# Optimization experiments

Hardware: AMD Instinct MI355X
Metric: run time of the kernel (lower is better)

## Reference

```python
import jax, jax.numpy as jnp
import numpy as np

B, T, IN, H, NC = 128, 256, 512, 1024, 10


def setup_inputs() -> dict:
    key = jax.random.key(0)
    ks = jax.random.split(key, 18)
    s = jnp.float32(0.05)

    def n(k, shape):
        return jax.random.normal(k, shape, dtype=jnp.float32) * s

    inp = {"x": n(ks[0], (B, T, IN))}
    in_dims = [IN, H, H]
    ki = 1
    for l in range(3):
        inp[f"w_ih{l}"] = n(ks[ki], (4 * H, in_dims[l])); ki += 1
        inp[f"w_hh{l}"] = n(ks[ki], (4 * H, H)); ki += 1
        inp[f"b_ih{l}"] = n(ks[ki], (4 * H,)); ki += 1
        inp[f"b_hh{l}"] = n(ks[ki], (4 * H,)); ki += 1
    inp["w1"] = n(ks[ki], (32, H)); ki += 1
    inp["b1"] = n(ks[ki], (32,)); ki += 1
    inp["w2"] = n(ks[ki], (NC, 32)); ki += 1
    inp["b2"] = n(ks[ki], (NC,))
    return inp


def _lstm_layer(xs, w_ih, w_hh, b):
    # xs: [B, T, D_in]; PyTorch gate order i, f, g, o
    bsz = xs.shape[0]
    hid = w_hh.shape[1]
    # Precompute input projection for all timesteps (one big GEMM)
    xp = jnp.einsum('bti,gi->btg', xs, w_ih) + b  # [B, T, 4H]

    def step(carry, xp_t):
        h, c = carry
        gates = xp_t + h @ w_hh.T  # [B, 4H]
        i, f, g, o = jnp.split(gates, 4, axis=-1)
        c = jax.nn.sigmoid(f) * c + jax.nn.sigmoid(i) * jnp.tanh(g)
        h = jax.nn.sigmoid(o) * jnp.tanh(c)
        return (h, c), h

    h0 = jnp.zeros((bsz, hid), xs.dtype)
    c0 = jnp.zeros((bsz, hid), xs.dtype)
    (_, _), hs = jax.lax.scan(step, (h0, c0), jnp.swapaxes(xp, 0, 1))
    return jnp.swapaxes(hs, 0, 1)  # [B, T, H]


def reference(x, w_ih0, w_hh0, b_ih0, b_hh0,
              w_ih1, w_hh1, b_ih1, b_hh1,
              w_ih2, w_hh2, b_ih2, b_hh2,
              w1, b1, w2, b2):
    h = x
    layers = [(w_ih0, w_hh0, b_ih0, b_hh0),
              (w_ih1, w_hh1, b_ih1, b_hh1),
              (w_ih2, w_hh2, b_ih2, b_hh2)]
    for w_ih, w_hh, b_ih, b_hh in layers:
        h = _lstm_layer(h, w_ih, w_hh, b_ih + b_hh)
    last = h[:, -1, :]                      # [B, H]
    hid = jax.nn.relu(last @ w1.T + b1)     # [B, 32]
    return hid @ w2.T + b2                  # [B, NC]
```

## Files before the change

kernel.cpp:

```cpp
#include <hip/hip_runtime.h>
#include <hip/hip_bf16.h>
#include <stdint.h>

#define B_ 128
#define T_ 256
#define IN_ 512
#define H_ 1024
#define G4_ 4096
#define TC_ 64
#define NCHUNK_ (T_ / TC_)

typedef __bf16 bf16x8 __attribute__((ext_vector_type(8)));
typedef float f32x4 __attribute__((ext_vector_type(4)));
typedef uint32_t u32x4 __attribute__((ext_vector_type(4)));

#define AS1U(p) ((const __attribute__((address_space(1))) unsigned int*)(p))
#define AS3U(p) ((__attribute__((address_space(3))) unsigned int*)(p))

__device__ __forceinline__ uint16_t f2bf(float f) {
  union { float f; uint32_t u; } v; v.f = f;
  uint32_t r = (v.u + 0x7fffu + ((v.u >> 16) & 1u)) >> 16;
  return (uint16_t)r;
}
__device__ __forceinline__ float bf2f(uint16_t h) {
  union { uint32_t u; float f; } v; v.u = ((uint32_t)h) << 16;
  return v.f;
}
__device__ __forceinline__ float sigmoid_f(float x) {
  return 1.f / (1.f + __expf(-x));
}
__device__ __forceinline__ float tanh_f(float x) {
  x = fminf(15.f, fmaxf(-15.f, x));
  float e = __expf(2.f * x);
  return (e - 1.f) / (e + 1.f);
}

__global__ void k_f32_to_bf16(const float* __restrict__ src, uint16_t* __restrict__ dst, int n) {
  int i = (blockIdx.x * blockDim.x + threadIdx.x) * 4;
  if (i >= n) return;
  float4 v = *(const float4*)(src + i);
  ushort4 o;
  o.x = f2bf(v.x); o.y = f2bf(v.y); o.z = f2bf(v.z); o.w = f2bf(v.w);
  *(ushort4*)(dst + i) = o;
}

__global__ void k_bias(const float* __restrict__ a, const float* __restrict__ b, float* __restrict__ o) {
  int i = blockIdx.x * blockDim.x + threadIdx.x;
  if (i < G4_) o[i] = a[i] + b[i];
}

__global__ void k_whh_frag(const float* __restrict__ whh, uint16_t* __restrict__ dst) {
  int t = blockIdx.x * blockDim.x + threadIdx.x;
  int lane = t & 63;
  int kk = (t >> 6) & 15;
  int w  = (t >> 10) & 15;
  int s5 = t >> 14;
  int nt = w & 7, kh = w >> 3;
  int row = (nt >> 1) * 1024 + s5 * 32 + (nt & 1) * 16 + (lane & 15);
  int col = kh * 512 + kk * 32 + ((lane >> 4) << 3);
  const float* sp = whh + (size_t)row * H_ + col;
  uint16_t o[8];
  #pragma unroll
  for (int j = 0; j < 8; ++j) o[j] = f2bf(sp[j]);
  uint4 pk;
  __builtin_memcpy(&pk, o, 16);
  *(uint4*)(dst + (size_t)t * 8) = pk;
}

__global__ __launch_bounds__(256, 1) void k_gemm_xp(
    const uint16_t* __restrict__ A, const uint16_t* __restrict__ W,
    const float* __restrict__ bias, uint16_t* __restrict__ xp,
    int K, int t0)
{
  __shared__ __align__(16) char smem[128 * 136 * 2];
  uint16_t* As = (uint16_t*)smem;
  uint16_t* Bs = (uint16_t*)(smem + 32768 / 2 * 2 - 16384);
  uint16_t* Cs = (uint16_t*)smem;
  const int tid = threadIdx.x;
  const int l = tid & 63;
  const int w = tid >> 6;
  const int mx = blockIdx.x;
  const int n0 = blockIdx.y * 128;
  const int wm = (w >> 1) * 64;
  const int wn = (w & 1) * 64;

  f32x4 acc[4][4] = {};

  for (int k0 = 0; k0 < K; k0 += 32) {
    __syncthreads();
    #pragma unroll
    for (int it = 0; it < 2; ++it) {
      const int chunk = w * 2 + it;
      const int loff = chunk * 1024 + l * 16;
      const int row = loff >> 6;
      const int colb = loff & 63;
      const int gm = mx * 512 + t0 + ((row >> 6) << 8) + (row & 63);
      const uint16_t* ga = A + (size_t)gm * K + k0 + (colb >> 1);
      __builtin_amdgcn_global_load_lds(AS1U(ga), AS3U((char*)As + chunk * 1024), 16, 0, 0);
      const uint16_t* gb = W + (size_t)(n0 + row) * K + k0 + (colb >> 1);
      __builtin_amdgcn_global_load_lds(AS1U(gb), AS3U((char*)Bs + chunk * 1024), 16, 0, 0);
    }
    __syncthreads();
    bf16x8 af[4], bfr[4];
    #pragma unroll
    for (int i = 0; i < 4; ++i)
      af[i] = *(const bf16x8*)&As[(wm + i * 16 + (l & 15)) * 32 + ((l >> 4) << 3)];
    #pragma unroll
    for (int j = 0; j < 4; ++j)
      bfr[j] = *(const bf16x8*)&Bs[(wn + j * 16 + (l & 15)) * 32 + ((l >> 4) << 3)];
    #pragma unroll
    for (int i = 0; i < 4; ++i) {
      #pragma unroll
      for (int j = 0; j < 4; ++j)
        acc[i][j] = __builtin_amdgcn_mfma_f32_16x16x32_bf16(af[i], bfr[j], acc[i][j], 0, 0, 0);
    }
  }
  __syncthreads();

  #pragma unroll
  for (int i = 0; i < 4; ++i) {
    const int row = wm + i * 16 + ((l >> 4) << 2);
    #pragma unroll
    for (int j = 0; j < 4; ++j) {
      const int col = wn + j * 16 + (l & 15);
      const float bv = bias[n0 + col];
      #pragma unroll
      for (int r = 0; r < 4; ++r)
        Cs[(row + r) * 136 + col] = f2bf(acc[i][j][r] + bv);
    }
  }
  __syncthreads();
  #pragma unroll
  for (int it = 0; it < 8; ++it) {
    const int row = it * 16 + w * 4 + (l >> 4);
    uint4 v = *(const uint4*)&Cs[row * 136 + (l & 15) * 8];
    *(uint4*)(xp + (size_t)(mx * 128 + row) * G4_ + n0 + (l & 15) * 8) = v;
  }
}

__global__ __launch_bounds__(1024, 4) void k_lstm(
    const uint16_t* __restrict__ whhf, const uint16_t* __restrict__ xp,
    uint16_t* __restrict__ seq, uint32_t* __restrict__ hbuf,
    float* __restrict__ cbuf, unsigned int* __restrict__ flags, int t0, int sall)
{
  __shared__ __align__(16) uint16_t Astg[2048 * 8];
  __shared__ float part[2][8][16][17];
  const int tid = threadIdx.x;
  const int l = tid & 63;
  const int w = tid >> 6;
  const int nt = w & 7;
  const int kh = w >> 3;
  const int bid = blockIdx.x;
  const int g = bid & 7;
  const int s5 = bid >> 3;
  const int U0 = s5 * 32;
  const int gs0 = g * 16;

  unsigned int* gflag = flags + g * 32;

  bf16x8 bfr[16];
  {
    const uint16_t* wp = whhf + (size_t)(s5 * 16 + w) * 8192 + l * 8;
    #pragma unroll
    for (int kk = 0; kk < 16; ++kk)
      bfr[kk] = *(const bf16x8*)(wp + kk * 512);
  }

  const int u = tid & 31;
  const int smg = (tid >> 5) & 15;
  float cc = 0.f;
  if (tid < 512) cc = cbuf[(size_t)(gs0 + smg) * H_ + U0 + u];

  uint16_t x0 = 0, x1 = 0, x2 = 0, x3 = 0;
  if (tid < 512) {
    const uint16_t* p = xp + ((size_t)(gs0 + smg) * TC_ + 0) * G4_ + U0 + u;
    x0 = p[0]; x1 = p[1024]; x2 = p[2048]; x3 = p[3072];
  }

  auto stage_fused = [&](int tl) {
    const int par = tl & 1;
    const unsigned tgt = (unsigned)tl;
    const char* src = (const char*)hbuf + (size_t)par * (B_ * H_ * 2)
                      + (size_t)(gs0 + w) * 2048 + (size_t)l * 32;
    const unsigned int* fp = gflag + (l >> 1);
    u32x4 q0, q1;
    unsigned fv;
    do {
      asm volatile(
        "global_load_dword %0, %3, off sc0 sc1\n\t"
        "global_load_dwordx4 %1, %4, off sc0 sc1\n\t"
        "global_load_dwordx4 %2, %4, off offset:16 sc0 sc1\n\t"
        "s_waitcnt vmcnt(0)"
        : "=&v"(fv), "=&v"(q0), "=&v"(q1)
        : "v"(fp), "v"(src)
        : "memory");
      if (fv >= tgt) break;
      __builtin_amdgcn_s_sleep(1);
    } while (true);
    const int base = 512 * l + ((w ^ (l & 7)) << 4);
    *(u32x4*)((char*)Astg + base) = q0;
    *(u32x4*)((char*)Astg + base + 256) = q1;
  };

  stage_fused(0);
  __syncthreads();

  for (int tl = 0; tl < TC_; ++tl) {
    const int par = tl & 1;

    f32x4 e0 = {0.f, 0.f, 0.f, 0.f};
    f32x4 e1 = {0.f, 0.f, 0.f, 0.f};
    #pragma unroll
    for (int kk = 0; kk < 16; kk += 2) {
      const int c0 = kh * 64 + kk * 4 + (l >> 4);
      const int c1 = c0 + 4;
      const int sw0 = (l & 15) ^ ((2 * kk + (l >> 5)) & 7);
      const int sw1 = (l & 15) ^ ((2 * (kk + 1) + (l >> 5)) & 7);
      bf16x8 a0 = *(const bf16x8*)((const char*)Astg + ((size_t)(c0 * 16 + sw0) << 4));
      bf16x8 a1 = *(const bf16x8*)((const char*)Astg + ((size_t)(c1 * 16 + sw1) << 4));
      e0 = __builtin_amdgcn_mfma_f32_16x16x32_bf16(a0, bfr[kk],     e0, 0, 0, 0);
      e1 = __builtin_amdgcn_mfma_f32_16x16x32_bf16(a1, bfr[kk + 1], e1, 0, 0, 0);
    }
    f32x4 e = e0 + e1;
    #pragma unroll
    for (int r = 0; r < 4; ++r)
      part[kh][nt][((l >> 4) << 2) + r][l & 15] = e[r];
    __syncthreads();

    if (tid < 512) {
      const int sub = u >> 4, uc = u & 15;
      float gi = part[0][0 + sub][smg][uc] + part[1][0 + sub][smg][uc] + bf2f(x0);
      float gf = part[0][2 + sub][smg][uc] + part[1][2 + sub][smg][uc] + bf2f(x1);
      float gg = part[0][4 + sub][smg][uc] + part[1][4 + sub][smg][uc] + bf2f(x2);
      float go = part[0][6 + sub][smg][uc] + part[1][6 + sub][smg][uc] + bf2f(x3);
      cc = sigmoid_f(gf) * cc + sigmoid_f(gi) * tanh_f(gg);
      float hh = sigmoid_f(go) * tanh_f(cc);
      uint16_t hb = f2bf(hh);
      unsigned int o = (unsigned int)__shfl_xor((int)(unsigned int)hb, 1);
      if ((u & 1) == 0) {
        uint32_t pk = (uint32_t)hb | (o << 16);
        const int b = gs0 + smg;
        uint32_t* hp = hbuf + (size_t)(1 - par) * (B_ * H_ / 2)
                            + ((size_t)b * H_ + U0 + u) / 2;
        __hip_atomic_store(hp, pk, __ATOMIC_RELAXED, __HIP_MEMORY_SCOPE_SYSTEM);
        if (sall || (t0 + tl == T_ - 1)) {
          uint32_t* sq = (uint32_t*)seq + (((size_t)b * T_ + (t0 + tl)) * H_ + U0 + u) / 2;
          *sq = pk;
        }
      }
      if (tl + 1 < TC_) {
        const uint16_t* p = xp + ((size_t)(gs0 + smg) * TC_ + tl + 1) * G4_ + U0 + u;
        x0 = p[0]; x1 = p[1024]; x2 = p[2048]; x3 = p[3072];
      }
    }
    __syncthreads();
    if (tid == 0)
      __hip_atomic_store(gflag + s5, (unsigned)(tl + 1),
                         __ATOMIC_RELAXED, __HIP_MEMORY_SCOPE_SYSTEM);
    if (tl + 1 < TC_) {
      stage_fused(tl + 1);
      __syncthreads();
    }
  }
  if (tid < 512) cbuf[(size_t)(gs0 + smg) * H_ + U0 + u] = cc;
}

__global__ __launch_bounds__(256) void k_mlp(
    const uint16_t* __restrict__ seq2,
    const float* __restrict__ w1, const float* __restrict__ b1,
    const float* __restrict__ w2, const float* __restrict__ b2,
    float* __restrict__ out)
{
  __shared__ float hv[H_];
  __shared__ float part[32][8];
  __shared__ float hid[32];
  const int b = blockIdx.x, tid = threadIdx.x;
  const uint16_t* hrow = seq2 + ((size_t)b * T_ + (T_ - 1)) * H_;
  for (int i = tid; i < H_; i += 256) hv[i] = bf2f(hrow[i]);
  __syncthreads();
  const int j = tid >> 3, p = tid & 7;
  float sum = 0.f;
  const float* wr = w1 + (size_t)j * H_ + p * 128;
  const float* hp = hv + p * 128;
  for (int k = 0; k < 128; ++k) sum += wr[k] * hp[k];
  part[j][p] = sum;
  __syncthreads();
  if (tid < 32) {
    float s2 = 0.f;
    #pragma unroll
    for (int pp = 0; pp < 8; ++pp) s2 += part[tid][pp];
    hid[tid] = fmaxf(s2 + b1[tid], 0.f);
  }
  __syncthreads();
  if (tid < 10) {
    float o = b2[tid];
    #pragma unroll
    for (int jj = 0; jj < 32; ++jj) o += hid[jj] * w2[tid * 32 + jj];
    out[b * 10 + tid] = o;
  }
}

extern "C" void kernel_launch(void* const* d_in, const int* in_sizes, int n_in,
                              void* d_out, int out_size, void* d_ws, size_t ws_size,
                              hipStream_t stream)
{
  const float* x = (const float*)d_in[0];
  const float* w_ih[3] = {(const float*)d_in[1], (const float*)d_in[5], (const float*)d_in[9]};
  const float* w_hh[3] = {(const float*)d_in[2], (const float*)d_in[6], (const float*)d_in[10]};
  const float* b_ih[3] = {(const float*)d_in[3], (const float*)d_in[7], (const float*)d_in[11]};
  const float* b_hh[3] = {(const float*)d_in[4], (const float*)d_in[8], (const float*)d_in[12]};
  const float* w1 = (const float*)d_in[13];
  const float* b1 = (const float*)d_in[14];
  const float* w2 = (const float*)d_in[15];
  const float* b2 = (const float*)d_in[16];
  float* out = (float*)d_out;

  char* ws = (char*)d_ws;
  size_t off = 0;
  auto alloc = [&](size_t bytes) {
    char* p = ws + off;
    off += (bytes + 255) & ~(size_t)255;
    return p;
  };
  uint16_t* XBF  = (uint16_t*)alloc((size_t)B_ * T_ * IN_ * 2);
  uint16_t* WIH0 = (uint16_t*)alloc((size_t)G4_ * IN_ * 2);
  uint16_t* WIH1 = (uint16_t*)alloc((size_t)G4_ * H_ * 2);
  uint16_t* WIH2 = (uint16_t*)alloc((size_t)G4_ * H_ * 2);
  float*    BIAS = (float*)alloc((size_t)3 * G4_ * 4);
  uint16_t* WHHF = (uint16_t*)alloc((size_t)3 * G4_ * H_ * 2);
  uint16_t* XP   = (uint16_t*)alloc((size_t)B_ * TC_ * G4_ * 2);
  uint16_t* SEQ  = (uint16_t*)alloc((size_t)B_ * T_ * H_ * 2);
  uint32_t* HBUF = (uint32_t*)alloc((size_t)2 * B_ * H_ * 2);
  float*    CBUF = (float*)alloc((size_t)B_ * H_ * 4);
  unsigned int* FLG = (unsigned int*)alloc((size_t)3 * NCHUNK_ * 1024 * 4);

  hipMemsetAsync(FLG, 0, (size_t)3 * NCHUNK_ * 1024 * 4, stream);

  int n;
  n = B_ * T_ * IN_;
  k_f32_to_bf16<<<n / 4 / 256, 256, 0, stream>>>(x, XBF, n);
  n = G4_ * IN_;
  k_f32_to_bf16<<<n / 4 / 256, 256, 0, stream>>>(w_ih[0], WIH0, n);
  n = G4_ * H_;
  k_f32_to_bf16<<<n / 4 / 256, 256, 0, stream>>>(w_ih[1], WIH1, n);
  k_f32_to_bf16<<<n / 4 / 256, 256, 0, stream>>>(w_ih[2], WIH2, n);
  for (int li = 0; li < 3; ++li)
    k_bias<<<16, 256, 0, stream>>>(b_ih[li], b_hh[li], BIAS + li * G4_);
  for (int li = 0; li < 3; ++li)
    k_whh_frag<<<2048, 256, 0, stream>>>(w_hh[li], WHHF + (size_t)li * G4_ * H_);

  const uint16_t* seq_in[3] = {XBF, SEQ, SEQ};
  const uint16_t* wih[3] = {WIH0, WIH1, WIH2};
  const int Ks[3] = {IN_, H_, H_};

  for (int li = 0; li < 3; ++li) {
    hipMemsetAsync(HBUF, 0, (size_t)2 * B_ * H_ * 2, stream);
    hipMemsetAsync(CBUF, 0, (size_t)B_ * H_ * 4, stream);
    const int sall = (li == 2) ? 0 : 1;
    for (int c = 0; c < NCHUNK_; ++c) {
      dim3 grid(64, 32);
      k_gemm_xp<<<grid, 256, 0, stream>>>(seq_in[li], wih[li], BIAS + li * G4_, XP,
                                          Ks[li], c * TC_);
      unsigned int* flg_lc = FLG + (size_t)(li * NCHUNK_ + c) * 1024;
      k_lstm<<<256, 1024, 0, stream>>>(WHHF + (size_t)li * G4_ * H_, XP, SEQ, HBUF,
                                       CBUF, flg_lc, c * TC_, sall);
    }
  }
  k_mlp<<<B_, 256, 0, stream>>>(SEQ, w1, b1, w2, b2, out);
}
```

Before: 3.312 ms.

## Overlap next-chunk input GEMM with LSTM recurrence in a fused kernel

Adds a fused kernel where the first 256 blocks run the LSTM recurrence for the current time chunk. The remaining blocks compute the input-projection GEMM for the next chunk into a second XP buffer, so the GEMM no longer sits serially between recurrence launches. The GEMM is retiled to 1024-thread blocks with 32x32 per-wave tiles, and it converts the fp32 input x to bf16 while loading, which removes the separate x conversion pass. The cost is that GEMM work now competes with the latency-bound recurrence for CU resources, and the launch bounds drop to two blocks per CU, which may change register allocation. A fallback keeps the serial schedule when the workspace is too small.

```diff
diff --git a/kernel.cpp b/kernel.cpp
--- a/kernel.cpp
+++ b/kernel.cpp
@@ -67,61 +67,72 @@
   *(uint4*)(dst + (size_t)t * 8) = pk;
 }
 
-__global__ __launch_bounds__(256, 1) void k_gemm_xp(
-    const uint16_t* __restrict__ A, const uint16_t* __restrict__ W,
-    const float* __restrict__ bias, uint16_t* __restrict__ xp,
-    int K, int t0)
-{
-  __shared__ __align__(16) char smem[128 * 136 * 2];
-  uint16_t* As = (uint16_t*)smem;
-  uint16_t* Bs = (uint16_t*)(smem + 32768 / 2 * 2 - 16384);
-  uint16_t* Cs = (uint16_t*)smem;
-  const int tid = threadIdx.x;
+__device__ __forceinline__ void gemm_body(
+    int tile, int tid, char* SM, const void* A, int Adt,
+    const uint16_t* __restrict__ W, const float* __restrict__ bias,
+    uint16_t* __restrict__ xp, int K, int t0)
+{
+  uint16_t* As = (uint16_t*)SM;
+  uint16_t* Bs = (uint16_t*)(SM + 8192);
+  uint16_t* Cs = (uint16_t*)SM;
   const int l = tid & 63;
   const int w = tid >> 6;
-  const int mx = blockIdx.x;
-  const int n0 = blockIdx.y * 128;
-  const int wm = (w >> 1) * 64;
-  const int wn = (w & 1) * 64;
-
-  f32x4 acc[4][4] = {};
+  const int mx = tile >> 5;
+  const int n0 = (tile & 31) << 7;
+  const int wm = (w >> 2) << 5;
+  const int wn = (w & 3) << 5;
+
+  f32x4 acc[2][2] = {};
 
   for (int k0 = 0; k0 < K; k0 += 32) {
     __syncthreads();
-    #pragma unroll
-    for (int it = 0; it < 2; ++it) {
-      const int chunk = w * 2 + it;
-      const int loff = chunk * 1024 + l * 16;
-      const int row = loff >> 6;
-      const int colb = loff & 63;
-      const int gm = mx * 512 + t0 + ((row >> 6) << 8) + (row & 63);
-      const uint16_t* ga = A + (size_t)gm * K + k0 + (colb >> 1);
-      __builtin_amdgcn_global_load_lds(AS1U(ga), AS3U((char*)As + chunk * 1024), 16, 0, 0);
+    if (w < 8) {
+      if (Adt == 0) {
+        const int loff = w * 1024 + l * 16;
+        const int row = loff >> 6, colb = loff & 63;
+        const int gm = mx * 512 + t0 + ((row >> 6) << 8) + (row & 63);
+        const uint16_t* ga = (const uint16_t*)A + (size_t)gm * K + k0 + (colb >> 1);
+        __builtin_amdgcn_global_load_lds(AS1U(ga), AS3U((char*)As + loff), 16, 0, 0);
+      } else {
+        const int idx = (w * 64 + l) * 8;
+        const int row = idx >> 5;
+        const int col = idx & 31;
+        const int gm = mx * 512 + t0 + ((row >> 6) << 8) + (row & 63);
+        const float* sp = (const float*)A + (size_t)gm * K + k0 + col;
+        float4 v0 = *(const float4*)sp;
+        float4 v1 = *(const float4*)(sp + 4);
+        uint16_t o[8] = {f2bf(v0.x), f2bf(v0.y), f2bf(v0.z), f2bf(v0.w),
+                         f2bf(v1.x), f2bf(v1.y), f2bf(v1.z), f2bf(v1.w)};
+        uint4 pk; __builtin_memcpy(&pk, o, 16);
+        *(uint4*)&As[row * 32 + col] = pk;
+      }
+    } else {
+      const int loff = (w - 8) * 1024 + l * 16;
+      const int row = loff >> 6, colb = loff & 63;
       const uint16_t* gb = W + (size_t)(n0 + row) * K + k0 + (colb >> 1);
-      __builtin_amdgcn_global_load_lds(AS1U(gb), AS3U((char*)Bs + chunk * 1024), 16, 0, 0);
+      __builtin_amdgcn_global_load_lds(AS1U(gb), AS3U((char*)Bs + loff), 16, 0, 0);
     }
     __syncthreads();
-    bf16x8 af[4], bfr[4];
-    #pragma unroll
-    for (int i = 0; i < 4; ++i)
+    bf16x8 af[2], bfr[2];
+    #pragma unroll
+    for (int i = 0; i < 2; ++i)
       af[i] = *(const bf16x8*)&As[(wm + i * 16 + (l & 15)) * 32 + ((l >> 4) << 3)];
     #pragma unroll
-    for (int j = 0; j < 4; ++j)
+    for (int j = 0; j < 2; ++j)
       bfr[j] = *(const bf16x8*)&Bs[(wn + j * 16 + (l & 15)) * 32 + ((l >> 4) << 3)];
     #pragma unroll
-    for (int i = 0; i < 4; ++i) {
+    for (int i = 0; i < 2; ++i)
       #pragma unroll
-      for (int j = 0; j < 4; ++j)
+      for (int j = 0; j < 2; ++j)
         acc[i][j] = __builtin_amdgcn_mfma_f32_16x16x32_bf16(af[i], bfr[j], acc[i][j], 0, 0, 0);
-    }
   }
   __syncthreads();
 
   #pragma unroll
-  for (int i = 0; i < 4; ++i) {
+  for (int i = 0; i < 2; ++i) {
     const int row = wm + i * 16 + ((l >> 4) << 2);
     #pragma unroll
-    for (int j = 0; j < 4; ++j) {
+    for (int j = 0; j < 2; ++j) {
       const int col = wn + j * 16 + (l & 15);
       const float bv = bias[n0 + col];
       #pragma unroll
@@ -131,26 +142,25 @@
   }
   __syncthreads();
   #pragma unroll
-  for (int it = 0; it < 8; ++it) {
-    const int row = it * 16 + w * 4 + (l >> 4);
-    uint4 v = *(const uint4*)&Cs[row * 136 + (l & 15) * 8];
-    *(uint4*)(xp + (size_t)(mx * 128 + row) * G4_ + n0 + (l & 15) * 8) = v;
-  }
-}
-
-__global__ __launch_bounds__(1024, 4) void k_lstm(
+  for (int p = 0; p < 2; ++p) {
+    const int row = p * 64 + (tid >> 4);
+    uint4 v = *(const uint4*)&Cs[row * 136 + (tid & 15) * 8];
+    *(uint4*)(xp + (size_t)(mx * 128 + row) * G4_ + n0 + (tid & 15) * 8) = v;
+  }
+}
+
+__device__ __forceinline__ void lstm_body(
+    int bid, int tid, char* SM,
     const uint16_t* __restrict__ whhf, const uint16_t* __restrict__ xp,
     uint16_t* __restrict__ seq, uint32_t* __restrict__ hbuf,
     float* __restrict__ cbuf, unsigned int* __restrict__ flags, int t0, int sall)
 {
-  __shared__ __align__(16) uint16_t Astg[2048 * 8];
-  __shared__ float part[2][8][16][17];
-  const int tid = threadIdx.x;
+  uint16_t* Astg = (uint16_t*)SM;
+  float (*part)[8][16][17] = (float(*)[8][16][17])(SM + 32768);
   const int l = tid & 63;
   const int w = tid >> 6;
   const int nt = w & 7;
   const int kh = w >> 3;
-  const int bid = blockIdx.x;
   const int g = bid & 7;
   const int s5 = bid >> 3;
   const int U0 = s5 * 32;
@@ -265,6 +275,31 @@
   if (tid < 512) cbuf[(size_t)(gs0 + smg) * H_ + U0 + u] = cc;
 }
 
+__global__ __launch_bounds__(1024, 2) void k_gemm(
+    const void* A, int Adt, const uint16_t* __restrict__ W,
+    const float* __restrict__ bias, uint16_t* __restrict__ xp, int K, int t0)
+{
+  __shared__ __align__(16) char SM[34816];
+  gemm_body(blockIdx.x, threadIdx.x, SM, A, Adt, W, bias, xp, K, t0);
+}
+
+__global__ __launch_bounds__(1024, 2) void k_fused(
+    const uint16_t* __restrict__ whhf, const uint16_t* __restrict__ xp_cur,
+    uint16_t* __restrict__ seq, uint32_t* __restrict__ hbuf,
+    float* __restrict__ cbuf, unsigned int* __restrict__ flags, int t0, int sall,
+    const void* gA, int Adt, const uint16_t* __restrict__ gW,
+    const float* __restrict__ gbias, uint16_t* __restrict__ xp_nxt,
+    int gK, int gt0, int ngemm)
+{
+  __shared__ __align__(16) char SM[50176];
+  const int bid = blockIdx.x;
+  if (bid < 256) {
+    lstm_body(bid, threadIdx.x, SM, whhf, xp_cur, seq, hbuf, cbuf, flags, t0, sall);
+  } else if (bid - 256 < ngemm) {
+    gemm_body(bid - 256, threadIdx.x, SM, gA, Adt, gW, gbias, xp_nxt, gK, gt0);
+  }
+}
+
 __global__ __launch_bounds__(256) void k_mlp(
     const uint16_t* __restrict__ seq2,
     const float* __restrict__ w1, const float* __restrict__ b1,
@@ -322,24 +357,23 @@
     off += (bytes + 255) & ~(size_t)255;
     return p;
   };
-  uint16_t* XBF  = (uint16_t*)alloc((size_t)B_ * T_ * IN_ * 2);
   uint16_t* WIH0 = (uint16_t*)alloc((size_t)G4_ * IN_ * 2);
   uint16_t* WIH1 = (uint16_t*)alloc((size_t)G4_ * H_ * 2);
   uint16_t* WIH2 = (uint16_t*)alloc((size_t)G4_ * H_ * 2);
   float*    BIAS = (float*)alloc((size_t)3 * G4_ * 4);
   uint16_t* WHHF = (uint16_t*)alloc((size_t)3 * G4_ * H_ * 2);
-  uint16_t* XP   = (uint16_t*)alloc((size_t)B_ * TC_ * G4_ * 2);
+  uint16_t* XPA  = (uint16_t*)alloc((size_t)B_ * TC_ * G4_ * 2);
   uint16_t* SEQ  = (uint16_t*)alloc((size_t)B_ * T_ * H_ * 2);
   uint32_t* HBUF = (uint32_t*)alloc((size_t)2 * B_ * H_ * 2);
   float*    CBUF = (float*)alloc((size_t)B_ * H_ * 4);
-  unsigned int* FLG = (unsigned int*)alloc((size_t)3 * NCHUNK_ * 1024 * 4);
-
-  hipMemsetAsync(FLG, 0, (size_t)3 * NCHUNK_ * 1024 * 4, stream);
-
-  int n;
-  n = B_ * T_ * IN_;
-  k_f32_to_bf16<<<n / 4 / 256, 256, 0, stream>>>(x, XBF, n);
-  n = G4_ * IN_;
+  unsigned int* FLG = (unsigned int*)alloc((size_t)12 * 1024 * 4);
+  const size_t need_pipe = off + (size_t)B_ * TC_ * G4_ * 2 + 4096;
+  const bool pipe = (ws_size >= need_pipe);
+  uint16_t* XPB = pipe ? (uint16_t*)alloc((size_t)B_ * TC_ * G4_ * 2) : XPA;
+
+  hipMemsetAsync(FLG, 0, (size_t)12 * 1024 * 4, stream);
+
+  int n = G4_ * IN_;
   k_f32_to_bf16<<<n / 4 / 256, 256, 0, stream>>>(w_ih[0], WIH0, n);
   n = G4_ * H_;
   k_f32_to_bf16<<<n / 4 / 256, 256, 0, stream>>>(w_ih[1], WIH1, n);
@@ -349,21 +383,53 @@
   for (int li = 0; li < 3; ++li)
     k_whh_frag<<<2048, 256, 0, stream>>>(w_hh[li], WHHF + (size_t)li * G4_ * H_);
 
-  const uint16_t* seq_in[3] = {XBF, SEQ, SEQ};
-  const uint16_t* wih[3] = {WIH0, WIH1, WIH2};
-  const int Ks[3] = {IN_, H_, H_};
-
-  for (int li = 0; li < 3; ++li) {
+  const void* gAsrc[3] = {(const void*)x, (const void*)SEQ, (const void*)SEQ};
+  const int   gAdt[3]  = {1, 0, 0};
+  const uint16_t* gWw[3] = {WIH0, WIH1, WIH2};
+  const int   gKk[3]   = {IN_, H_, H_};
+
+  if (pipe) {
     hipMemsetAsync(HBUF, 0, (size_t)2 * B_ * H_ * 2, stream);
     hipMemsetAsync(CBUF, 0, (size_t)B_ * H_ * 4, stream);
-    const int sall = (li == 2) ? 0 : 1;
-    for (int c = 0; c < NCHUNK_; ++c) {
-      dim3 grid(64, 32);
-      k_gemm_xp<<<grid, 256, 0, stream>>>(seq_in[li], wih[li], BIAS + li * G4_, XP,
-                                          Ks[li], c * TC_);
-      unsigned int* flg_lc = FLG + (size_t)(li * NCHUNK_ + c) * 1024;
-      k_lstm<<<256, 1024, 0, stream>>>(WHHF + (size_t)li * G4_ * H_, XP, SEQ, HBUF,
-                                       CBUF, flg_lc, c * TC_, sall);
+    k_gemm<<<2048, 1024, 0, stream>>>(gAsrc[0], gAdt[0], gWw[0], BIAS, XPA, gKk[0], 0);
+    uint16_t* xpb[2] = {XPA, XPB};
+    for (int k = 0; k < 12; ++k) {
+      const int li = k >> 2, c = k & 3;
+      if (c == 0 && k > 0) {
+        hipMemsetAsync(HBUF, 0, (size_t)2 * B_ * H_ * 2, stream);
+        hipMemsetAsync(CBUF, 0, (size_t)B_ * H_ * 4, stream);
+      }
+      const int sall = (li == 2) ? 0 : 1;
+      unsigned int* flg = FLG + (size_t)k * 1024;
+      if (k < 11) {
+        const int kn = k + 1, lj = kn >> 2, cj = kn & 3;
+        k_fused<<<2304, 1024, 0, stream>>>(
+            WHHF + (size_t)li * G4_ * H_, xpb[k & 1], SEQ, HBUF, CBUF, flg,
+            c * TC_, sall,
+            gAsrc[lj], gAdt[lj], gWw[lj], BIAS + lj * G4_, xpb[kn & 1],
+            gKk[lj], cj * TC_, 2048);
+      } else {
+        k_fused<<<256, 1024, 0, stream>>>(
+            WHHF + (size_t)li * G4_ * H_, xpb[k & 1], SEQ, HBUF, CBUF, flg,
+            c * TC_, sall,
+            nullptr, 0, nullptr, nullptr, nullptr, 0, 0, 0);
+      }
+    }
+  } else {
+    for (int k = 0; k < 12; ++k) {
+      const int li = k >> 2, c = k & 3;
+      if (c == 0) {
+        hipMemsetAsync(HBUF, 0, (size_t)2 * B_ * H_ * 2, stream);
+        hipMemsetAsync(CBUF, 0, (size_t)B_ * H_ * 4, stream);
+      }
+      const int sall = (li == 2) ? 0 : 1;
+      unsigned int* flg = FLG + (size_t)k * 1024;
+      k_gemm<<<2048, 1024, 0, stream>>>(gAsrc[li], gAdt[li], gWw[li],
+                                        BIAS + li * G4_, XPA, gKk[li], c * TC_);
+      k_fused<<<256, 1024, 0, stream>>>(
+          WHHF + (size_t)li * G4_ * H_, XPA, SEQ, HBUF, CBUF, flg,
+          c * TC_, sall,
+          nullptr, 0, nullptr, nullptr, nullptr, 0, 0, 0);
     }
   }
   k_mlp<<<B_, 256, 0, stream>>>(SEQ, w1, b1, w2, b2, out);
```

After: 4.291 ms. 1.3x slower.
